# Kernel tuning notes

Measured on AMD Instinct MI355X. Metric: run time of the kernel, lower is better.

## Reference

```python
import jax, jax.numpy as jnp
import numpy as np

EPS_WN = 1e-6
EPS_BN = 1e-5

def wn_linear(x, W):
    # WeightNormlinear with scale=False, bias=False: y = (x W^T) / ||W_row||
    norm = jnp.sqrt(jnp.sum(W * W, axis=1) + EPS_WN)  # [out]
    return (x @ W.T) / norm

def hyper_weights(z, W0, W2, W3):
    # z: [N_O, N_I, E] -> conv weight [N_O*16, N_I*16, 3, 3], bias [N_O*16]
    N_O, N_I, E = z.shape
    bias = wn_linear(z.reshape(N_O, N_I * E), W0).reshape(-1)      # [N_O*16]
    w = wn_linear(z, W2).reshape(N_O, N_I, 16, E)                  # fc2
    w = wn_linear(w, W3)                                           # fc3 -> [N_O,N_I,16,16*9]
    w = w.reshape(N_O, N_I, 16, 16, 3, 3).transpose(0, 2, 1, 3, 4, 5)
    w = w.reshape(N_O * 16, N_I * 16, 3, 3)
    return jnp.sign(w), jnp.sign(bias)  # BinarizeWF forward

def conv3x3(x, w, stride):
    return jax.lax.conv_general_dilated(
        x, w, (stride, stride), ((1, 1), (1, 1)),
        dimension_numbers=('NCHW', 'OIHW', 'NCHW'))

def batchnorm(x, gamma, beta):
    # training-mode BN: biased batch statistics over (N,H,W)
    mean = jnp.mean(x, axis=(0, 2, 3), keepdims=True)
    var = jnp.var(x, axis=(0, 2, 3), keepdims=True)
    return gamma[None, :, None, None] * (x - mean) * jax.lax.rsqrt(var + EPS_BN) + beta[None, :, None, None]

def setup_inputs() -> dict:
    key = jax.random.key(0)
    ks = jax.random.split(key, 10)
    B, C, H, W = 16, 256, 56, 56
    E = 64
    NO = NI = C // 16
    def uni(k, shape, s):
        return jax.random.uniform(k, shape, jnp.float32, -s, s)
    stdv_z = 5.0 / np.sqrt(E)          # random_z init
    stdv0 = 4.0 / np.sqrt(E * NI)      # fc0: in = E*N_I
    stdv23 = 4.0 / np.sqrt(E)          # fc2/fc3: in = E
    return {
        'x': jax.random.normal(ks[0], (B, C, H, W), jnp.float32),
        'z1': uni(ks[1], (NO, NI, E), stdv_z),
        'W0_1': uni(ks[2], (16, E * NI), stdv0),
        'W2_1': uni(ks[3], (16 * E, E), stdv23),
        'W3_1': uni(ks[4], (16 * 9, E), stdv23),
        'gamma1': jnp.ones((C,), jnp.float32),
        'beta1': jnp.zeros((C,), jnp.float32),
        'z2': uni(ks[5], (NO, NO, E), stdv_z),
        'W0_2': uni(ks[6], (16, E * NO), stdv0),
        'W2_2': uni(ks[7], (16 * E, E), stdv23),
        'W3_2': uni(ks[8], (16 * 9, E), stdv23),
        'gamma2': jnp.ones((C,), jnp.float32),
        'beta2': jnp.zeros((C,), jnp.float32),
    }

def reference(x, z1, W0_1, W2_1, W3_1, gamma1, beta1,
              z2, W0_2, W2_2, W3_2, gamma2, beta2):
    residual = x
    # conv1 (stride=1): binarize activations (C != 3), hyper-generated binary weights
    w1, b1 = hyper_weights(z1, W0_1, W2_1, W3_1)
    out = conv3x3(jnp.sign(x), w1, 1) + b1[None, :, None, None]
    out = batchnorm(out, gamma1, beta1)
    # conv2
    w2, b2 = hyper_weights(z2, W0_2, W2_2, W3_2)
    out2 = conv3x3(jnp.sign(out), w2, 1) + b2[None, :, None, None]
    out2 = batchnorm(out2, gamma2, beta2)
    return out2 + residual
```

## Files before the change

kernel.cpp:

```cpp
#include <hip/hip_runtime.h>
#include <stdint.h>

typedef int v4i __attribute__((ext_vector_type(4)));
typedef int v16i __attribute__((ext_vector_type(16)));



__global__ __launch_bounds__(256, 2) void fused_pre_kernel(
    const float* __restrict__ z1, const float* __restrict__ W21,
    const float* __restrict__ W31, const float* __restrict__ z2,
    const float* __restrict__ W22, const float* __restrict__ W32,
    int8_t* __restrict__ Wb1, int8_t* __restrict__ Wb2,
    const float* __restrict__ W01, const float* __restrict__ W02,
    int* __restrict__ b1, int* __restrict__ b2,
    unsigned long long* __restrict__ sums,
    const float* __restrict__ x, int8_t* __restrict__ Sp) {
  __shared__ __align__(16) float Wt[16384];
  __shared__ __align__(16) float hbuf[16 * 72];
  __shared__ __align__(16) float zsh[64];
  __shared__ __align__(16) int8_t pk[2304];
  const int tid = threadIdx.x;

  if (blockIdx.x >= 545) {
    const int fs = blockIdx.x - 545;
    const int xcd = blockIdx.x & 7;
    const int orig = xcd * 116 + (fs >> 3);
    const int b = orig / 58, h = orig % 58;
    int8_t* rowp = Sp + ((size_t)b * 58 + h) * 58 * 256;
    if (h == 0 || h == 57) {
      #pragma unroll
      for (int i = 0; i < 4; ++i) {
        int idx = i * 256 + tid;
        if (idx < 928) *(v4i*)(rowp + (size_t)idx * 16) = (v4i){0, 0, 0, 0};
      }
      return;
    }
    int8_t* t = (int8_t*)Wt;
    const float* xb = x + (size_t)b * 802816 + (size_t)(h - 1) * 56;
    for (int i = 0; i < 56; ++i) {
      int flat = i * 256 + tid;
      int c = flat / 56, w = flat - c * 56;
      float v = xb[(size_t)c * 3136 + w];
      t[w * 256 + (c ^ ((w & 31) << 3))] = (v > 0.f) ? 1 : ((v < 0.f) ? -1 : 0);
    }
    if (tid < 32) {
      int col = tid >> 4;
      *(v4i*)(rowp + (col ? 57 * 256 : 0) + (tid & 15) * 16) = (v4i){0, 0, 0, 0};
    }
    __syncthreads();
    int8_t* dst = rowp + 256;
    for (int i = 0; i < 7; ++i) {
      int f8 = i * 256 + tid;
      int w = f8 >> 5, c0 = (f8 & 31) << 3;
      uint2 v = *(const uint2*)&t[w * 256 + (c0 ^ ((w & 31) << 3))];
      *(uint2*)(dst + (size_t)w * 256 + c0) = v;
    }
    return;
  }

  if (blockIdx.x >= 512) {
    const int pb = blockIdx.x - 512;
    if (pb == 32) {
      #pragma unroll
      for (int i = 0; i < 4; ++i) sums[i * 256 + tid] = 0ull;
      return;
    }
    float* zs = Wt;
    const int set = pb >> 4, o = pb & 15;
    const float* z = set ? z2 : z1;
    const float* W0 = set ? W02 : W01;
    int* bout = set ? b2 : b1;
    #pragma unroll
    for (int i = 0; i < 4; ++i) zs[i * 256 + tid] = z[(size_t)o * 1024 + i * 256 + tid];
    __syncthreads();
    const int j = tid >> 4, l = tid & 15;
    const float* wr = W0 + (size_t)j * 1024;
    double acc = 0.0;
    #pragma unroll 4
    for (int it = 0; it < 16; ++it) {
      float4 w4 = *(const float4*)&wr[it * 64 + l * 4];
      float4 z4 = *(const float4*)&zs[it * 64 + l * 4];
      acc += (double)w4.x * z4.x + (double)w4.y * z4.y + (double)w4.z * z4.z + (double)w4.w * z4.w;
    }
    #pragma unroll
    for (int m = 1; m < 16; m <<= 1) acc += __shfl_xor(acc, m, 64);
    if (l == 0) bout[o * 16 + j] = (acc > 0.0) ? 1 : ((acc < 0.0) ? -1 : 0);
    return;
  }

  const int set = blockIdx.x >> 8;
  const int oi = blockIdx.x & 255;
  const float* z = set ? z2 : z1;
  const float* W2 = set ? W22 : W21;
  const float* W3 = set ? W32 : W31;
  int8_t* Wb = set ? Wb2 : Wb1;

  if (tid < 16) *(float4*)&zsh[tid * 4] = ((const float4*)(z + (size_t)oi * 64))[tid];
  __syncthreads();

  const int key2 = (tid ^ (tid >> 4)) & 15;
  for (int c = 0; c < 4; ++c) {
    if (c) __syncthreads();
    const float4* src = (const float4*)W2 + c * 4096;
    #pragma unroll
    for (int i = 0; i < 16; ++i) {
      int G = i * 256 + tid;
      int row = G >> 4, g = G & 15;
      *(float4*)&Wt[row * 64 + (((g ^ row ^ (row >> 4)) & 15) << 2)] = src[G];
    }
    __syncthreads();
    double ax = 0, ay = 0, az = 0, aw = 0;
    double nx = 0, ny = 0, nz = 0, nw = 0;
    #pragma unroll
    for (int it = 0; it < 16; ++it) {
      float4 w4 = *(const float4*)&Wt[tid * 64 + ((it ^ key2) << 2)];
      float4 z4 = *(const float4*)&zsh[it * 4];
      ax += (double)w4.x * z4.x; ay += (double)w4.y * z4.y;
      az += (double)w4.z * z4.z; aw += (double)w4.w * z4.w;
      nx += (double)w4.x * w4.x; ny += (double)w4.y * w4.y;
      nz += (double)w4.z * w4.z; nw += (double)w4.w * w4.w;
    }
    double dot = (ax + ay) + (az + aw);
    double ss = (nx + ny) + (nz + nw);
    int j = c * 256 + tid;
    hbuf[(j >> 6) * 72 + (j & 63)] = (float)(dot / sqrt(ss + 1e-6));
  }
  __syncthreads();

  {
    const float4* src = (const float4*)W3;
    #pragma unroll
    for (int i = 0; i < 9; ++i) {
      int G = i * 256 + tid;
      int row = G >> 4, g = G & 15;
      *(float4*)&Wt[row * 64 + (((g ^ row ^ (row >> 4)) & 15) << 2)] = src[G];
    }
  }
  __syncthreads();

  {
    const int q = tid >> 4, sub = tid & 15;
    #pragma unroll
    for (int k = 0; k < 9; ++k) {
      int jj = sub + (k << 4);
      const int key3 = (sub ^ k) & 15;
      double ax = 0, ay = 0, az = 0, aw = 0;
      #pragma unroll
      for (int it = 0; it < 16; ++it) {
        float4 w4 = *(const float4*)&Wt[jj * 64 + ((it ^ key3) << 2)];
        float4 h4 = *(const float4*)&hbuf[q * 72 + it * 4];
        ax += (double)w4.x * h4.x; ay += (double)w4.y * h4.y;
        az += (double)w4.z * h4.z; aw += (double)w4.w * h4.w;
      }
      double acc = (ax + ay) + (az + aw);
      int8_t sgn = (acc > 0.0) ? (int8_t)1 : ((acc < 0.0) ? (int8_t)(-1) : (int8_t)0);
      int tp = jj / 9, tap = jj - tp * 9;
      pk[tap * 256 + q * 16 + tp] = sgn;
    }
  }
  __syncthreads();

  if (tid < 144) {
    const int tap = tid >> 4, qq = tid & 15;
    const int o = oi >> 4, ii = oi & 15;
    const int chunk = ((tap << 2) + (ii >> 2)) * 2 + ((ii >> 1) & 1);
    v4i val = *(const v4i*)&pk[tap * 256 + qq * 16];
    *(v4i*)(Wb + (size_t)chunk * 8192 + (size_t)(o * 16 + qq) * 32 + ((ii & 1) << 4)) = val;
  }
}


template <int MODE>
__global__ __launch_bounds__(512, 4) void conv_kernel(
    const int8_t* __restrict__ Sp, const int16_t* __restrict__ rawin,
    const unsigned long long* __restrict__ sumsIn,
    const float* __restrict__ gamma, const float* __restrict__ beta,
    const int8_t* __restrict__ WbP, const int* __restrict__ bias,
    int16_t* __restrict__ raw, unsigned long long* __restrict__ sumsOut)
{
  __shared__ __align__(16) int8_t lds[59392];
  __shared__ float thrS[256];
  __shared__ int sfS[256];
  const int tid = threadIdx.x;
  const int lane = tid & 63;
  const int f0 = blockIdx.x + 28 * blockIdx.y;
  const int orig = (f0 & 7) * 56 + (f0 >> 3);
  const int b = orig / 28, bx = orig % 28;
  const int H0 = bx << 1;

  const int n = lane & 31, kg = lane >> 5;
  const int wid = tid >> 6;
  const int cogrp = wid & 3, pxgrp = wid >> 2;

  if (MODE == 1) {
    if (tid < 256) {
      double S = (double)(long long)sumsIn[tid];
      double Q = (double)(long long)sumsIn[256 + tid];
      double mean = S / 50176.0;
      double var = Q / 50176.0 - mean * mean;
      double istd = 1.0 / sqrt(var + 1e-5);
      double A = (double)gamma[tid] * istd;
      float Af = (float)A;
      float thr; int sf;
      if (Af > 0.f)      { thr = (float)(mean - (double)beta[tid] / A); sf = 1; }
      else if (Af < 0.f) { thr = (float)(mean - (double)beta[tid] / A); sf = -1; }
      else               { thr = -1e30f; sf = (beta[tid] > 0.f) ? 1 : ((beta[tid] < 0.f) ? -1 : 0); }
      thrS[tid] = thr; sfS[tid] = sf;
    }
    __syncthreads();
  }

  const int8_t* Abase = WbP + (size_t)((cogrp << 6) + n) * 32 + (kg << 4);
  v4i Ar[2][2][2];
  #pragma unroll
  for (int c2 = 0; c2 < 2; ++c2)
    #pragma unroll
    for (int a = 0; a < 2; ++a)
      Ar[0][c2][a] = *(const v4i*)(Abase + (size_t)c2 * 8192 + a * 1024);

  if (MODE == 0) {
    const int8_t* SpB = Sp + ((size_t)b * 58 + H0) * 58 * 256;
    #pragma unroll
    for (int ph = 0; ph < 2; ++ph) {
      v4i tmp[4];
      #pragma unroll
      for (int it = 0; it < 4; ++it) {
        int G = (ph * 4 + it) * 512 + tid;
        if (G < 3712) {
          int pp = G >> 4, gl = G & 15;
          int wp = pp % 58;
          tmp[it] = *(const v4i*)(SpB + pp * 256 + ((gl ^ (wp & 7)) << 4));
        }
      }
      #pragma unroll
      for (int it = 0; it < 4; ++it) {
        int G = (ph * 4 + it) * 512 + tid;
        if (G < 3712) *(v4i*)(lds + (G << 4)) = tmp[it];
      }
    }
  } else {
    const int gsrc = tid & 15;
    const int ppt = tid >> 4;
    float thr[16]; int sf[16];
    #pragma unroll
    for (int j = 0; j < 16; ++j) { thr[j] = thrS[gsrc * 16 + j]; sf[j] = sfS[gsrc * 16 + j]; }
    #pragma unroll
    for (int it = 0; it < 8; ++it) {
      int pp = it * 32 + ppt;
      if (pp < 232) {
        int prow = pp / 58, pcol = pp - prow * 58;
        int ir = H0 + prow - 1, ic = pcol - 1;
        v4i outv = (v4i){0, 0, 0, 0};
        if (ir >= 0 && ir <= 55 && ic >= 0 && ic <= 55) {
          const int16_t* src = rawin + ((size_t)(b * 3136 + ir * 56 + ic)) * 256 + gsrc * 16;
          v4i lo = *(const v4i*)src;
          v4i hi = *(const v4i*)(src + 8);
          #pragma unroll
          for (int j = 0; j < 16; ++j) {
            int wd = (j < 8) ? lo[(j >> 1) & 3] : hi[(j >> 1) & 3];
            int v = (j & 1) ? (wd >> 16) : (int)(short)wd;
            float fv = (float)v;
            int bj = (fv > thr[j]) ? sf[j] : ((fv < thr[j]) ? -sf[j] : 0);
            outv[j >> 2] |= (bj & 0xff) << ((j & 3) << 3);
          }
        }
        *(v4i*)(lds + ((pp << 4) + (gsrc ^ (pcol & 7))) * 16) = outv;
      }
    }
  }

  int pixoff[2], wcol[2];
  #pragma unroll
  for (int f = 0; f < 2; ++f) {
    int px = (((pxgrp << 1) + f) << 5) + n;
    if (px > 111) px = 111;
    int hh = px / 56, ww = px - hh * 56;
    pixoff[f] = hh * 58 + ww;
    wcol[f] = ww;
  }

  v16i acc[2][2];
  #pragma unroll
  for (int f = 0; f < 2; ++f)
    #pragma unroll
    for (int a = 0; a < 2; ++a)
      #pragma unroll
      for (int e = 0; e < 16; ++e) acc[f][a][e] = 0;

  __syncthreads();

  #pragma unroll
  for (int ks = 0; ks < 36; ++ks) {
    const int cur = ks & 1;
    if (ks + 1 < 36) {
      #pragma unroll
      for (int c2 = 0; c2 < 2; ++c2)
        #pragma unroll
        for (int a = 0; a < 2; ++a)
          Ar[cur ^ 1][c2][a] = *(const v4i*)(Abase + (size_t)((ks + 1) * 2 + c2) * 8192 + a * 1024);
    }
    const int tap = ks >> 2, c64 = ks & 3;
    const int r = tap / 3, s = tap - 3 * (tap / 3);
    #pragma unroll
    for (int c2 = 0; c2 < 2; ++c2) {
      v4i Af0 = Ar[cur][c2][0], Af1 = Ar[cur][c2][1];
      #pragma unroll
      for (int f = 0; f < 2; ++f) {
        const int gb = (c64 << 2) + (c2 << 1) + kg;
        v4i Bf = *(const v4i*)(lds + ((pixoff[f] + r * 58 + s) << 8)
                               + ((gb ^ ((wcol[f] + s) & 7)) << 4));
        acc[f][0] = __builtin_amdgcn_mfma_i32_32x32x32_i8(Af0, Bf, acc[f][0], 0, 0, 0);
        acc[f][1] = __builtin_amdgcn_mfma_i32_32x32x32_i8(Af1, Bf, acc[f][1], 0, 0, 0);
      }
    }
  }

  __syncthreads();
  #pragma unroll
  for (int f = 0; f < 2; ++f) {
    int px = (((pxgrp << 1) + f) << 5) + n;
    if (px < 112) {
      #pragma unroll
      for (int a = 0; a < 2; ++a) {
        #pragma unroll
        for (int q = 0; q < 4; ++q) {
          int co = (cogrp << 6) + (a << 5) + (q << 3) + (kg << 2);
          v4i bi = *(const v4i*)(bias + co);
          short4 o;
          o.x = (short)(acc[f][a][q * 4 + 0] + bi.x);
          o.y = (short)(acc[f][a][q * 4 + 1] + bi.y);
          o.z = (short)(acc[f][a][q * 4 + 2] + bi.z);
          o.w = (short)(acc[f][a][q * 4 + 3] + bi.w);
          int g = co >> 3;
          *(short4*)(lds + px * 512 + ((g ^ (px & 31)) << 4) + (kg << 3)) = o;
        }
      }
    }
  }
  __syncthreads();
  const int pbase = b * 3136 + bx * 112;
  const int gg = tid & 31;
  int s8[8], q8[8];
  #pragma unroll
  for (int j = 0; j < 8; ++j) { s8[j] = 0; q8[j] = 0; }
  #pragma unroll
  for (int i = 0; i < 7; ++i) {
    int rrow = i * 16 + (tid >> 5);
    v4i val = *(const v4i*)(lds + rrow * 512 + ((gg ^ (rrow & 31)) << 4));
    *(v4i*)(raw + (size_t)(pbase + rrow) * 256 + gg * 8) = val;
    #pragma unroll
    for (int j = 0; j < 8; ++j) {
      int wd = val[j >> 1];
      int v = (j & 1) ? (wd >> 16) : (int)(short)wd;
      s8[j] += v; q8[j] += v * v;
    }
  }
  __syncthreads();
  int* red = (int*)lds;
  #pragma unroll
  for (int j = 0; j < 8; ++j) { red[tid * 8 + j] = s8[j]; red[4096 + tid * 8 + j] = q8[j]; }
  __syncthreads();
  if (tid < 256) {
    const int ch = tid;
    const int own = ch >> 3, sub = ch & 7;
    long long S = 0, Q = 0;
    #pragma unroll
    for (int jj = 0; jj < 16; ++jj) {
      int t2 = own + 32 * jj;
      S += red[t2 * 8 + sub];
      Q += red[4096 + t2 * 8 + sub];
    }
    atomicAdd(&sumsOut[ch], (unsigned long long)S);
    atomicAdd(&sumsOut[256 + ch], (unsigned long long)Q);
  }
}


__global__ void final_kernel(const int16_t* __restrict__ raw2,
                             const unsigned long long* __restrict__ sums2,
                             const float* __restrict__ gamma, const float* __restrict__ beta,
                             const float* __restrict__ x, float* __restrict__ out) {
  __shared__ float t[256 * 57];
  __shared__ __align__(16) float mS[256], AS[256], bS[256];
  const int tid = threadIdx.x;
  const int f0 = blockIdx.x + 56 * blockIdx.y;
  const int orig = (f0 & 7) * 112 + (f0 >> 3);
  const int b = orig / 56, h = orig % 56;
  const int rowp = b * 3136 + h * 56;
  {
    double S = (double)(long long)sums2[tid];
    double Q = (double)(long long)sums2[256 + tid];
    double mean = S / 50176.0;
    double var = Q / 50176.0 - mean * mean;
    double istd = 1.0 / sqrt(var + 1e-5);
    mS[tid] = (float)mean;
    AS[tid] = gamma[tid] * (float)istd;
    bS[tid] = beta[tid];
  }
  __syncthreads();
  for (int i = 0; i < 7; ++i) {
    int f8 = i * 256 + tid;
    int px = f8 >> 5, c0 = (f8 & 31) << 3;
    float m[8], A[8], bb[8];
    *(float4*)&m[0]  = *(const float4*)&mS[c0];
    *(float4*)&m[4]  = *(const float4*)&mS[c0 + 4];
    *(float4*)&A[0]  = *(const float4*)&AS[c0];
    *(float4*)&A[4]  = *(const float4*)&AS[c0 + 4];
    *(float4*)&bb[0] = *(const float4*)&bS[c0];
    *(float4*)&bb[4] = *(const float4*)&bS[c0 + 4];
    v4i vv = *(const v4i*)(raw2 + (size_t)(rowp + px) * 256 + c0);
    #pragma unroll
    for (int j = 0; j < 8; ++j) {
      int wd = vv[j >> 1];
      int v = (j & 1) ? (wd >> 16) : (int)(short)wd;
      t[(c0 + j) * 57 + px] = ((float)v - m[j]) * A[j] + bb[j];
    }
  }
  __syncthreads();
  const float* xb = x + (size_t)b * 802816 + (size_t)h * 56;
  float* ob = out + (size_t)b * 802816 + (size_t)h * 56;
  for (int i = 0; i < 16; ++i) {
    int idx = i * 256 + tid;
    int c = idx >> 4, wq = idx & 15;
    if (wq < 14) {
      int w0 = wq * 4;
      float4 xv = *(const float4*)(xb + (size_t)c * 3136 + w0);
      float4 o;
      o.x = t[c * 57 + w0 + 0] + xv.x;
      o.y = t[c * 57 + w0 + 1] + xv.y;
      o.z = t[c * 57 + w0 + 2] + xv.z;
      o.w = t[c * 57 + w0 + 3] + xv.w;
      *(float4*)(ob + (size_t)c * 3136 + w0) = o;
    }
  }
}


extern "C" void kernel_launch(void* const* d_in, const int* in_sizes, int n_in,
                              void* d_out, int out_size, void* d_ws, size_t ws_size,
                              hipStream_t stream) {
  const float* x      = (const float*)d_in[0];
  const float* z1     = (const float*)d_in[1];
  const float* W0_1   = (const float*)d_in[2];
  const float* W2_1   = (const float*)d_in[3];
  const float* W3_1   = (const float*)d_in[4];
  const float* gamma1 = (const float*)d_in[5];
  const float* beta1  = (const float*)d_in[6];
  const float* z2     = (const float*)d_in[7];
  const float* W0_2   = (const float*)d_in[8];
  const float* W2_2   = (const float*)d_in[9];
  const float* W3_2   = (const float*)d_in[10];
  const float* gamma2 = (const float*)d_in[11];
  const float* beta2  = (const float*)d_in[12];
  float* out = (float*)d_out;

  char* ws = (char*)d_ws;
  size_t off = 0;
  auto alloc = [&](size_t sz) -> void* {
    void* p = ws + off;
    off += (sz + 255) & ~(size_t)255;
    return p;
  };
  int8_t* Sp1   = (int8_t*)alloc(13778944);
  int16_t* raw1 = (int16_t*)alloc(25690112);
  int16_t* raw2 = (int16_t*)alloc(25690112);
  int8_t* Wb1   = (int8_t*)alloc(589824);
  int8_t* Wb2   = (int8_t*)alloc(589824);
  int* b1       = (int*)alloc(1024);
  int* b2       = (int*)alloc(1024);
  unsigned long long* sums = (unsigned long long*)alloc(8192);
  if (ws_size < off) return;

  fused_pre_kernel<<<1473, 256, 0, stream>>>(z1, W2_1, W3_1, z2, W2_2, W3_2, Wb1, Wb2,
                                             W0_1, W0_2, b1, b2, sums, x, Sp1);
  conv_kernel<0><<<dim3(28, 16), 512, 0, stream>>>(Sp1, nullptr, nullptr, nullptr, nullptr,
                                                   Wb1, b1, raw1, sums);
  conv_kernel<1><<<dim3(28, 16), 512, 0, stream>>>(nullptr, raw1, sums, gamma1, beta1,
                                                   Wb2, b2, raw2, sums + 512);
  final_kernel<<<dim3(56, 16), 256, 0, stream>>>(raw2, sums + 512, gamma2, beta2, x, out);
}
```

Before: 172.3 us.

## Halve hypernetwork weight LDS tile to raise pre-kernel occupancy

Shrinks the shared W tile in the fused pre-kernel from 64KB to 32KB. The fc2 stage now loads W2 in 8 chunks and splits each row's 64-element dot across two thread halves, combining the halves through shared double buffers. The fc3 stage loads W3 in two halves. This lets three blocks fit per CU instead of two, at the cost of more barriers and chunked loads. The fc3 accumulation order in double precision changes slightly.

New measurement: 158.7 us (median of 2 runs). -7.9%, faster.

```diff
diff --git a/kernel.cpp b/kernel.cpp
--- a/kernel.cpp
+++ b/kernel.cpp
@@ -6,7 +6,7 @@
 
 
 
-__global__ __launch_bounds__(256, 2) void fused_pre_kernel(
+__global__ __launch_bounds__(256, 3) void fused_pre_kernel(
     const float* __restrict__ z1, const float* __restrict__ W21,
     const float* __restrict__ W31, const float* __restrict__ z2,
     const float* __restrict__ W22, const float* __restrict__ W32,
@@ -15,7 +15,9 @@
     int* __restrict__ b1, int* __restrict__ b2,
     unsigned long long* __restrict__ sums,
     const float* __restrict__ x, int8_t* __restrict__ Sp) {
-  __shared__ __align__(16) float Wt[16384];
+  __shared__ __align__(16) float Wt[8192];
+  __shared__ __align__(16) double pdot[256];
+  __shared__ __align__(16) double pnrm[256];
   __shared__ __align__(16) float hbuf[16 * 72];
   __shared__ __align__(16) float zsh[64];
   __shared__ __align__(16) int8_t pk[2304];
@@ -98,64 +100,75 @@
   if (tid < 16) *(float4*)&zsh[tid * 4] = ((const float4*)(z + (size_t)oi * 64))[tid];
   __syncthreads();
 
-  const int key2 = (tid ^ (tid >> 4)) & 15;
-  for (int c = 0; c < 4; ++c) {
-    if (c) __syncthreads();
-    const float4* src = (const float4*)W2 + c * 4096;
-    #pragma unroll
-    for (int i = 0; i < 16; ++i) {
-      int G = i * 256 + tid;
-      int row = G >> 4, g = G & 15;
-      *(float4*)&Wt[row * 64 + (((g ^ row ^ (row >> 4)) & 15) << 2)] = src[G];
-    }
-    __syncthreads();
-    double ax = 0, ay = 0, az = 0, aw = 0;
-    double nx = 0, ny = 0, nz = 0, nw = 0;
-    #pragma unroll
-    for (int it = 0; it < 16; ++it) {
-      float4 w4 = *(const float4*)&Wt[tid * 64 + ((it ^ key2) << 2)];
-      float4 z4 = *(const float4*)&zsh[it * 4];
-      ax += (double)w4.x * z4.x; ay += (double)w4.y * z4.y;
-      az += (double)w4.z * z4.z; aw += (double)w4.w * z4.w;
-      nx += (double)w4.x * w4.x; ny += (double)w4.y * w4.y;
-      nz += (double)w4.z * w4.z; nw += (double)w4.w * w4.w;
-    }
-    double dot = (ax + ay) + (az + aw);
-    double ss = (nx + ny) + (nz + nw);
-    int j = c * 256 + tid;
-    hbuf[(j >> 6) * 72 + (j & 63)] = (float)(dot / sqrt(ss + 1e-6));
-  }
-  __syncthreads();
-
   {
-    const float4* src = (const float4*)W3;
-    #pragma unroll
-    for (int i = 0; i < 9; ++i) {
-      int G = i * 256 + tid;
-      int row = G >> 4, g = G & 15;
-      *(float4*)&Wt[row * 64 + (((g ^ row ^ (row >> 4)) & 15) << 2)] = src[G];
-    }
-  }
-  __syncthreads();
+    const int r = tid & 127, half = tid >> 7;
+    for (int c = 0; c < 8; ++c) {
+      if (c) __syncthreads();
+      const float4* src = (const float4*)W2 + (size_t)c * 2048;
+      #pragma unroll
+      for (int i = 0; i < 8; ++i) {
+        int G = i * 256 + tid;
+        int row = G >> 4, g = G & 15;
+        *(float4*)&Wt[row * 64 + (((g ^ row ^ (row >> 4)) & 15) << 2)] = src[G];
+      }
+      __syncthreads();
+      double ax = 0, ay = 0, az = 0, aw = 0;
+      double nx = 0, ny = 0, nz = 0, nw = 0;
+      #pragma unroll
+      for (int it = 0; it < 8; ++it) {
+        int gi = half * 8 + it;
+        float4 w4 = *(const float4*)&Wt[r * 64 + (((gi ^ r ^ (r >> 4)) & 15) << 2)];
+        float4 z4 = *(const float4*)&zsh[gi * 4];
+        ax += (double)w4.x * z4.x; ay += (double)w4.y * z4.y;
+        az += (double)w4.z * z4.z; aw += (double)w4.w * z4.w;
+        nx += (double)w4.x * w4.x; ny += (double)w4.y * w4.y;
+        nz += (double)w4.z * w4.z; nw += (double)w4.w * w4.w;
+      }
+      pdot[tid] = (ax + ay) + (az + aw);
+      pnrm[tid] = (nx + ny) + (nz + nw);
+      __syncthreads();
+      if (tid < 128) {
+        double dot = pdot[tid] + pdot[tid + 128];
+        double ss  = pnrm[tid] + pnrm[tid + 128];
+        int j = c * 128 + tid;
+        hbuf[(j >> 6) * 72 + (j & 63)] = (float)(dot / sqrt(ss + 1e-6));
+      }
+    }
+  }
 
   {
     const int q = tid >> 4, sub = tid & 15;
     #pragma unroll
-    for (int k = 0; k < 9; ++k) {
-      int jj = sub + (k << 4);
-      const int key3 = (sub ^ k) & 15;
-      double ax = 0, ay = 0, az = 0, aw = 0;
-      #pragma unroll
-      for (int it = 0; it < 16; ++it) {
-        float4 w4 = *(const float4*)&Wt[jj * 64 + ((it ^ key3) << 2)];
-        float4 h4 = *(const float4*)&hbuf[q * 72 + it * 4];
-        ax += (double)w4.x * h4.x; ay += (double)w4.y * h4.y;
-        az += (double)w4.z * h4.z; aw += (double)w4.w * h4.w;
-      }
-      double acc = (ax + ay) + (az + aw);
-      int8_t sgn = (acc > 0.0) ? (int8_t)1 : ((acc < 0.0) ? (int8_t)(-1) : (int8_t)0);
-      int tp = jj / 9, tap = jj - tp * 9;
-      pk[tap * 256 + q * 16 + tp] = sgn;
+    for (int h = 0; h < 2; ++h) {
+      __syncthreads();
+      const float4* src = (const float4*)W3 + h * 1152;
+      #pragma unroll
+      for (int i = 0; i < 5; ++i) {
+        int G = i * 256 + tid;
+        if (G < 1152) {
+          int lr = G >> 4, g = G & 15;
+          *(float4*)&Wt[lr * 64 + (((g ^ lr ^ (lr >> 4)) & 15) << 2)] = src[G];
+        }
+      }
+      __syncthreads();
+      #pragma unroll
+      for (int k = 0; k < 9; ++k) {
+        int jj = sub + (k << 4);
+        if (jj >= h * 72 && jj < h * 72 + 72) {
+          int lr = jj - h * 72;
+          double a = 0.0;
+          #pragma unroll
+          for (int it = 0; it < 16; ++it) {
+            float4 w4 = *(const float4*)&Wt[lr * 64 + (((it ^ lr ^ (lr >> 4)) & 15) << 2)];
+            float4 h4 = *(const float4*)&hbuf[q * 72 + it * 4];
+            a += (double)w4.x * h4.x + (double)w4.y * h4.y
+               + (double)w4.z * h4.z + (double)w4.w * h4.w;
+          }
+          int8_t sgn = (a > 0.0) ? (int8_t)1 : ((a < 0.0) ? (int8_t)(-1) : (int8_t)0);
+          int tp = jj / 9, tap = jj - tp * 9;
+          pk[tap * 256 + q * 16 + tp] = sgn;
+        }
+      }
     }
   }
   __syncthreads();
```
